# Optimization experiments

Hardware: AMD Instinct MI355X
Metric: run time of the kernel (lower is better)

Reference implementation:

```python
import jax, jax.numpy as jnp
import numpy as np

K_SIZE = 5  # pred_k_size


def setup_inputs() -> dict:
    key = jax.random.key(0)
    k1, k2 = jax.random.split(key)
    bs, c, h, w = 4, 64, 160, 160
    fm = jax.random.normal(k1, (bs, c, h, w), dtype=jnp.float32)
    kernel = jax.random.normal(k2, (bs, K_SIZE * K_SIZE, h, w), dtype=jnp.float32)
    return {"fm": fm, "kernel": kernel, "dilation": 1}


def reference(fm, kernel, dilation):
    # fm: [bs, c, h, w]; kernel: [bs, k*k, h, w]
    bs, c, h, w = fm.shape
    k = K_SIZE
    pad = (k // 2) * dilation
    feat_padded = jnp.pad(fm, ((0, 0), (0, 0), (pad, pad), (pad, pad)))
    kern = jnp.flip(kernel, axis=1)  # torch.flip(kernel, dims=[1])
    # stack k*k shifted views: [bs, k*k, c, h, w]
    img_stack = jnp.stack(
        [
            feat_padded[:, :, i * dilation:i * dilation + h, j * dilation:j * dilation + w]
            for i in range(k)
            for j in range(k)
        ],
        axis=1,
    )
    # per-pixel weighted sum over the k*k taps -> [bs, c, h, w]
    res = jnp.sum(kern[:, :, None, :, :] * img_stack, axis=1)
    return res
```

## Files before the change

kernel.cpp:

```cpp
#include <hip/hip_runtime.h>

#define K   5
#define KK  25
#define H   160
#define W   160
#define C   64
#define BS  4
#define HW  (H * W)
#define CPG 4
#define BLK 256

__global__ __launch_bounds__(BLK) void kconv_kernel(
    const float* __restrict__ fm,
    const float* __restrict__ kern,
    const int*  __restrict__ dil,
    float* __restrict__ out)
{
    const int q  = blockIdx.x * BLK + threadIdx.x;
    const int b  = blockIdx.z;
    const int cg = blockIdx.y;
    const int d  = dil[0];

    const int y = q / (W / 4);
    const int x = (q - y * (W / 4)) * 4;

    const float* fb = fm  + ((size_t)b * C + (size_t)cg * CPG) * HW;
    float*       ob = out + ((size_t)b * C + (size_t)cg * CPG) * HW + (size_t)y * W + x;
    const float* kb = kern + (size_t)b * KK * HW + (size_t)y * W + x;

    if (d == 1) {
        float acc[CPG][4];
#pragma unroll
        for (int c = 0; c < CPG; ++c)
#pragma unroll
            for (int p = 0; p < 4; ++p) acc[c][p] = 0.f;

        const int a_col = (x >= 2) ? (x - 2) : 0;
        const int d_col = (x + 4 <= W - 2) ? (x + 4) : (W - 2);

#pragma unroll
        for (int i = 0; i < K; ++i) {
            const int  yy  = y + i - 2;
            const bool rok = (yy >= 0) && (yy < H);
            const int  yr  = rok ? yy : 0;

            float wrow[K][4];
#pragma unroll
            for (int j = 0; j < K; ++j) {
                const int t = i * K + j;
                const float4 wv = *(const float4*)(kb + (size_t)(KK - 1 - t) * HW);
                const float wf[4] = {wv.x, wv.y, wv.z, wv.w};
#pragma unroll
                for (int p = 0; p < 4; ++p) {
                    const int col = x + p + j - 2;
                    const bool ok = rok && (col >= 0) && (col < W);
                    wrow[j][p] = ok ? wf[p] : 0.f;
                }
            }

            const float* rowbase = fb + (size_t)yr * W;
            float win[CPG][8];
#pragma unroll
            for (int c = 0; c < CPG; ++c) {
                const float* r = rowbase + (size_t)c * HW;
                const float2 A  = *(const float2*)(r + a_col);
                const float2 Bv = *(const float2*)(r + x);
                const float2 Cv = *(const float2*)(r + x + 2);
                const float2 Dv = *(const float2*)(r + d_col);
                win[c][0] = A.x;  win[c][1] = A.y;
                win[c][2] = Bv.x; win[c][3] = Bv.y;
                win[c][4] = Cv.x; win[c][5] = Cv.y;
                win[c][6] = Dv.x; win[c][7] = Dv.y;
            }

#pragma unroll
            for (int c = 0; c < CPG; ++c)
#pragma unroll
                for (int j = 0; j < K; ++j)
#pragma unroll
                    for (int p = 0; p < 4; ++p)
                        acc[c][p] = fmaf(wrow[j][p], win[c][p + j], acc[c][p]);
        }

#pragma unroll
        for (int c = 0; c < CPG; ++c) {
            const float4 o = {acc[c][0], acc[c][1], acc[c][2], acc[c][3]};
            *(float4*)(ob + (size_t)c * HW) = o;
        }
    } else {
#pragma unroll 1
        for (int p = 0; p < 4; ++p) {
            const int xx = x + p;
            float wgt[KK];
            int   offs[KK];
#pragma unroll 1
            for (int i = 0; i < K; ++i) {
                const int  yy  = y + (i - 2) * d;
                const bool yok = (yy >= 0) && (yy < H);
                const int  yc  = min(max(yy, 0), H - 1);
#pragma unroll 1
                for (int j = 0; j < K; ++j) {
                    const int  xc  = xx + (j - 2) * d;
                    const bool ok  = yok && (xc >= 0) && (xc < W);
                    const int  xcc = min(max(xc, 0), W - 1);
                    const int  t   = i * K + j;
                    wgt[t]  = ok ? kb[(size_t)(KK - 1 - t) * HW + p] : 0.f;
                    offs[t] = yc * W + xcc;
                }
            }
#pragma unroll 1
            for (int c = 0; c < CPG; ++c) {
                const float* fc = fb + (size_t)c * HW;
                float a2 = 0.f;
#pragma unroll 1
                for (int t = 0; t < KK; ++t) a2 = fmaf(wgt[t], fc[offs[t]], a2);
                ob[(size_t)c * HW + p] = a2;
            }
        }
    }
}

extern "C" void kernel_launch(void* const* d_in, const int* in_sizes, int n_in,
                              void* d_out, int out_size, void* d_ws, size_t ws_size,
                              hipStream_t stream)
{
    const float* fm   = (const float*)d_in[0];
    const float* kern = (const float*)d_in[1];
    const int*   dil  = (const int*)d_in[2];
    float*       out  = (float*)d_out;

    dim3 grid(HW / 4 / BLK, C / CPG, BS);
    kconv_kernel<<<grid, dim3(BLK), 0, stream>>>(fm, kern, dil, out);
}
```

Measured before the change: 107.6 us.

## Stage feature halo tiles and per-pixel weights in LDS for 2D block tiles

```diff
diff --git a/kernel.cpp b/kernel.cpp
--- a/kernel.cpp
+++ b/kernel.cpp
@@ -1,14 +1,22 @@
 #include <hip/hip_runtime.h>
 
-#define K   5
-#define KK  25
-#define H   160
-#define W   160
-#define C   64
-#define BS  4
-#define HW  (H * W)
-#define CPG 4
-#define BLK 256
+#define K    5
+#define KK   25
+#define H    160
+#define W    160
+#define C    64
+#define BS   4
+#define HW   (H * W)
+
+#define TX   32
+#define TY   8
+#define CPB  16
+#define CPW  4
+#define BLK  256
+
+#define FR   (TY + 4)
+#define FS   44
+#define WLS  36
 
 __global__ __launch_bounds__(BLK) void kconv_kernel(
     const float* __restrict__ fm,
@@ -16,78 +24,93 @@
     const int*  __restrict__ dil,
     float* __restrict__ out)
 {
-    const int q  = blockIdx.x * BLK + threadIdx.x;
-    const int b  = blockIdx.z;
-    const int cg = blockIdx.y;
-    const int d  = dil[0];
+    __shared__ float fmlds[CPB * FR * FS];
+    __shared__ float wlds[KK * TY * WLS];
 
-    const int y = q / (W / 4);
-    const int x = (q - y * (W / 4)) * 4;
+    const int tid   = threadIdx.x;
+    const int x0    = blockIdx.x * TX;
+    const int y0    = blockIdx.y * TY;
+    const int b     = blockIdx.z >> 2;
+    const int cg    = blockIdx.z & 3;
+    const int cbase = cg * CPB;
+    const int d     = dil[0];
 
-    const float* fb = fm  + ((size_t)b * C + (size_t)cg * CPG) * HW;
-    float*       ob = out + ((size_t)b * C + (size_t)cg * CPG) * HW + (size_t)y * W + x;
-    const float* kb = kern + (size_t)b * KK * HW + (size_t)y * W + x;
+    const int lane = tid & 63;
+    const int qx   = lane & 7;
+    const int ty   = lane >> 3;
+    const int c0   = (tid >> 6) * CPW;
 
     if (d == 1) {
-        float acc[CPG][4];
+        const float* fmb = fm + ((size_t)b * C + cbase) * HW;
+        for (int idx = tid; idx < CPB * FR * 10; idx += BLK) {
+            const int ch  = idx / (FR * 10);
+            const int rem = idx - ch * (FR * 10);
+            const int r   = rem / 10;
+            const int f4  = rem - r * 10;
+            const int gy  = y0 - 2 + r;
+            const int gx  = x0 - 4 + 4 * f4;
+            float4 v = make_float4(0.f, 0.f, 0.f, 0.f);
+            if (gy >= 0 && gy < H && gx >= 0 && gx < W)
+                v = *(const float4*)(fmb + (size_t)ch * HW + (size_t)gy * W + gx);
+            *(float4*)&fmlds[(ch * FR + r) * FS + 4 * f4] = v;
+        }
+        const float* kb = kern + (size_t)b * KK * HW + (size_t)y0 * W + x0;
+        for (int idx = tid; idx < KK * TY * 8; idx += BLK) {
+            const int m   = idx / (TY * 8);
+            const int rem = idx - m * (TY * 8);
+            const int r   = rem / 8;
+            const int f4  = rem - r * 8;
+            const float4 v = *(const float4*)(kb + (size_t)m * HW + (size_t)r * W + 4 * f4);
+            *(float4*)&wlds[((KK - 1 - m) * TY + r) * WLS + 4 * f4] = v;
+        }
+        __syncthreads();
+
+        float acc[CPW][4];
 #pragma unroll
-        for (int c = 0; c < CPG; ++c)
+        for (int c = 0; c < CPW; ++c)
 #pragma unroll
             for (int p = 0; p < 4; ++p) acc[c][p] = 0.f;
 
-        const int a_col = (x >= 2) ? (x - 2) : 0;
-        const int d_col = (x + 4 <= W - 2) ? (x + 4) : (W - 2);
-
 #pragma unroll
         for (int i = 0; i < K; ++i) {
-            const int  yy  = y + i - 2;
-            const bool rok = (yy >= 0) && (yy < H);
-            const int  yr  = rok ? yy : 0;
-
-            float wrow[K][4];
+            float wr[K][4];
 #pragma unroll
             for (int j = 0; j < K; ++j) {
-                const int t = i * K + j;
-                const float4 wv = *(const float4*)(kb + (size_t)(KK - 1 - t) * HW);
-                const float wf[4] = {wv.x, wv.y, wv.z, wv.w};
+                const float4 wv = *(const float4*)&wlds[((i * K + j) * TY + ty) * WLS + 4 * qx];
+                wr[j][0] = wv.x; wr[j][1] = wv.y; wr[j][2] = wv.z; wr[j][3] = wv.w;
+            }
+            float win[CPW][8];
 #pragma unroll
-                for (int p = 0; p < 4; ++p) {
-                    const int col = x + p + j - 2;
-                    const bool ok = rok && (col >= 0) && (col < W);
-                    wrow[j][p] = ok ? wf[p] : 0.f;
+            for (int c = 0; c < CPW; ++c) {
+                const int base = ((c0 + c) * FR + ty + i) * FS + 4 * qx + 2;
+#pragma unroll
+                for (int k = 0; k < 4; ++k) {
+                    const float2 t = *(const float2*)&fmlds[base + 2 * k];
+                    win[c][2 * k]     = t.x;
+                    win[c][2 * k + 1] = t.y;
                 }
             }
-
-            const float* rowbase = fb + (size_t)yr * W;
-            float win[CPG][8];
 #pragma unroll
-            for (int c = 0; c < CPG; ++c) {
-                const float* r = rowbase + (size_t)c * HW;
-                const float2 A  = *(const float2*)(r + a_col);
-                const float2 Bv = *(const float2*)(r + x);
-                const float2 Cv = *(const float2*)(r + x + 2);
-                const float2 Dv = *(const float2*)(r + d_col);
-                win[c][0] = A.x;  win[c][1] = A.y;
-                win[c][2] = Bv.x; win[c][3] = Bv.y;
-                win[c][4] = Cv.x; win[c][5] = Cv.y;
-                win[c][6] = Dv.x; win[c][7] = Dv.y;
-            }
-
-#pragma unroll
-            for (int c = 0; c < CPG; ++c)
+            for (int c = 0; c < CPW; ++c)
 #pragma unroll
                 for (int j = 0; j < K; ++j)
 #pragma unroll
                     for (int p = 0; p < 4; ++p)
-                        acc[c][p] = fmaf(wrow[j][p], win[c][p + j], acc[c][p]);
+                        acc[c][p] = fmaf(wr[j][p], win[c][p + j], acc[c][p]);
         }
 
+        float* ob = out + ((size_t)b * C + cbase + c0) * HW + (size_t)(y0 + ty) * W + x0 + 4 * qx;
 #pragma unroll
-        for (int c = 0; c < CPG; ++c) {
+        for (int c = 0; c < CPW; ++c) {
             const float4 o = {acc[c][0], acc[c][1], acc[c][2], acc[c][3]};
             *(float4*)(ob + (size_t)c * HW) = o;
         }
     } else {
+        const int x = x0 + 4 * qx;
+        const int y = y0 + ty;
+        const float* fb  = fm  + ((size_t)b * C + cbase + c0) * HW;
+        float*       ob  = out + ((size_t)b * C + cbase + c0) * HW + (size_t)y * W + x;
+        const float* kbp = kern + (size_t)b * KK * HW + (size_t)y * W + x;
 #pragma unroll 1
         for (int p = 0; p < 4; ++p) {
             const int xx = x + p;
@@ -104,12 +127,12 @@
                     const bool ok  = yok && (xc >= 0) && (xc < W);
                     const int  xcc = min(max(xc, 0), W - 1);
                     const int  t   = i * K + j;
-                    wgt[t]  = ok ? kb[(size_t)(KK - 1 - t) * HW + p] : 0.f;
+                    wgt[t]  = ok ? kbp[(size_t)(KK - 1 - t) * HW + p] : 0.f;
                     offs[t] = yc * W + xcc;
                 }
             }
 #pragma unroll 1
-            for (int c = 0; c < CPG; ++c) {
+            for (int c = 0; c < CPW; ++c) {
                 const float* fc = fb + (size_t)c * HW;
                 float a2 = 0.f;
 #pragma unroll 1
@@ -129,6 +152,6 @@
     const int*   dil  = (const int*)d_in[2];
     float*       out  = (float*)d_out;
 
-    dim3 grid(HW / 4 / BLK, C / CPG, BS);
+    dim3 grid(W / TX, H / TY, BS * (C / CPB));
     kconv_kernel<<<grid, dim3(BLK), 0, stream>>>(fm, kern, dil, out);
 }
```

Result: slower. 115.8 us (+7.7%).
